# Kernel optimization log

Hardware: AMD Instinct MI355X
Metric: run time of the kernel (lower is better)

## Reference

```python
import math
import jax, jax.numpy as jnp
import numpy as np

B, S, D, H = 8, 1024, 1024, 16
P_DROP = 0.1  # dropout prob p used in forward
NEG_INF = -1e20


def setup_inputs() -> dict:
    key = jax.random.key(0)
    kq, kk, kv, km, kd = jax.random.split(key, 5)
    query = jax.random.normal(kq, (B, S, D), dtype=jnp.float32)
    key_t = jax.random.normal(kk, (B, S, D), dtype=jnp.float32)
    value = jax.random.normal(kv, (B, S, D), dtype=jnp.float32)
    mask = jax.random.randint(km, (B, S), 0, 2, dtype=jnp.int32)
    # Bernoulli keep-mask, as produced by an external dropout layer
    dropout_mask = (jax.random.uniform(kd, (B * H, S, S)) > P_DROP).astype(jnp.float32)
    return {"query": query, "key": key_t, "value": value,
            "mask": mask, "dropout_mask": dropout_mask}


def reference(query, key, value, mask, dropout_mask):
    b, q_len, dim = query.shape
    k_len = key.shape[1]
    dph = dim // H
    scale = math.sqrt(dph)

    def split_heads(t):  # [b, s, dim] -> [b, H, s, dph]
        return t.reshape(b, t.shape[1], H, dph).transpose(0, 2, 1, 3)

    q = split_heads(query) / scale
    k = split_heads(key)
    v = split_heads(value)

    # [b, H, q, k]
    scores = jnp.einsum('bhqd,bhkd->bhqk', q, k)
    attn_mask = (mask == 0)[:, None, None, :]  # [b,1,1,k]
    scores = jnp.where(attn_mask, NEG_INF, scores)

    # softmax in float32, cast back to query dtype
    weights = jax.nn.softmax(scores.astype(jnp.float32), axis=-1).astype(query.dtype)
    weights = weights * dropout_mask.reshape(b, H, q_len, k_len) * (1.0 / (1.0 - P_DROP))

    out = jnp.einsum('bhqk,bhkd->bhqd', weights, v)  # [b,H,q,dph]
    return out.transpose(0, 2, 1, 3).reshape(b, q_len, dim)
```

## Files before the change

### kernel.cpp

```cpp
#include <hip/hip_runtime.h>

namespace {
constexpr int Bn = 8;
constexpr int Sn = 1024;
constexpr int Dn = 1024;
constexpr int Hn = 16;
constexpr int DPH = 64;
constexpr int QB  = 64;
constexpr int KB  = 64;
constexpr float QSCALE    = 0.125f;
constexpr float DROPSCALE = 1.0f / 0.9f;

typedef __attribute__((ext_vector_type(4))) float    f32x4;
typedef __attribute__((ext_vector_type(8))) _Float16 f16x8;
typedef __attribute__((ext_vector_type(4))) _Float16 f16x4;
}

__global__ __launch_bounds__(256)
void mha_fwd(const float* __restrict__ Q, const float* __restrict__ K,
             const float* __restrict__ V, const int* __restrict__ msk,
             const float* __restrict__ dmask, float* __restrict__ out)
{
    __shared__ __align__(16) _Float16 Ql[QB][DPH + 8];
    __shared__ __align__(16) _Float16 Kl[KB][DPH + 8];
    __shared__ __align__(16) _Float16 Vt[DPH][KB + 8];
    __shared__ __align__(16) _Float16 Pl[4][16][KB + 8];

    const int tid = threadIdx.x;
    const int w   = tid >> 6;
    const int l   = tid & 63;
    const int fr  = l & 15;
    const int kg  = (l >> 4) << 3;
    const int rg  = (l >> 4) << 2;

    const int bid = blockIdx.x;
    const int qt = bid & (Sn / QB - 1);
    const int h  = (bid >> 4) & (Hn - 1);
    const int b  = bid >> 8;
    const int qbase = qt * QB;

    {
        const int row = tid >> 2;
        const int seg = (tid & 3) << 4;
        const float4* gq = reinterpret_cast<const float4*>(
            Q + ((size_t)(b * Sn + qbase + row)) * Dn + h * DPH + seg);
        #pragma unroll
        for (int i = 0; i < 4; ++i) {
            float4 v = gq[i];
            f16x4 qp;
            qp[0] = (_Float16)(v.x * QSCALE);
            qp[1] = (_Float16)(v.y * QSCALE);
            qp[2] = (_Float16)(v.z * QSCALE);
            qp[3] = (_Float16)(v.w * QSCALE);
            *reinterpret_cast<f16x4*>(&Ql[row][seg + i * 4]) = qp;
        }
    }
    __syncthreads();

    f16x8 qf0 = *reinterpret_cast<const f16x8*>(&Ql[w * 16 + fr][kg]);
    f16x8 qf1 = *reinterpret_cast<const f16x8*>(&Ql[w * 16 + fr][32 + kg]);

    f32x4 acc[4];
    #pragma unroll
    for (int dt = 0; dt < 4; ++dt) acc[dt] = (f32x4){0.f, 0.f, 0.f, 0.f};
    float m_r[4] = {-INFINITY, -INFINITY, -INFINITY, -INFINITY};
    float l_r[4] = {0.f, 0.f, 0.f, 0.f};

    const float* dm_base = dmask + ((size_t)(b * Hn + h)) * Sn * Sn
                         + (size_t)(qbase + w * 16) * Sn;

    #pragma unroll 1
    for (int kt = 0; kt < Sn / KB; ++kt) {
        __syncthreads();
        {
            const int row = tid >> 2;
            const int seg = (tid & 3) << 4;
            const size_t goff = ((size_t)(b * Sn + kt * KB + row)) * Dn + h * DPH + seg;
            const float4* gk = reinterpret_cast<const float4*>(K + goff);
            const float4* gv = reinterpret_cast<const float4*>(V + goff);
            #pragma unroll
            for (int i = 0; i < 4; ++i) {
                float4 kv = gk[i];
                f16x4 kp;
                kp[0] = (_Float16)kv.x; kp[1] = (_Float16)kv.y;
                kp[2] = (_Float16)kv.z; kp[3] = (_Float16)kv.w;
                *reinterpret_cast<f16x4*>(&Kl[row][seg + i * 4]) = kp;
                float4 vv = gv[i];
                Vt[seg + i * 4 + 0][row] = (_Float16)vv.x;
                Vt[seg + i * 4 + 1][row] = (_Float16)vv.y;
                Vt[seg + i * 4 + 2][row] = (_Float16)vv.z;
                Vt[seg + i * 4 + 3][row] = (_Float16)vv.w;
            }
        }
        __syncthreads();

        f32x4 sc[4];
        #pragma unroll
        for (int ct = 0; ct < 4; ++ct) {
            f16x8 kf0 = *reinterpret_cast<const f16x8*>(&Kl[ct * 16 + fr][kg]);
            f16x8 kf1 = *reinterpret_cast<const f16x8*>(&Kl[ct * 16 + fr][32 + kg]);
            f32x4 z = {0.f, 0.f, 0.f, 0.f};
            z = __builtin_amdgcn_mfma_f32_16x16x32_f16(qf0, kf0, z, 0, 0, 0);
            z = __builtin_amdgcn_mfma_f32_16x16x32_f16(qf1, kf1, z, 0, 0, 0);
            sc[ct] = z;
        }
        #pragma unroll
        for (int ct = 0; ct < 4; ++ct) {
            if (msk[b * Sn + kt * KB + ct * 16 + fr] == 0) {
                #pragma unroll
                for (int r = 0; r < 4; ++r) sc[ct][r] = -1e20f;
            }
        }
        float tm[4];
        #pragma unroll
        for (int r = 0; r < 4; ++r)
            tm[r] = fmaxf(fmaxf(sc[0][r], sc[1][r]), fmaxf(sc[2][r], sc[3][r]));
        #pragma unroll
        for (int off = 1; off < 16; off <<= 1) {
            #pragma unroll
            for (int r = 0; r < 4; ++r)
                tm[r] = fmaxf(tm[r], __shfl_xor(tm[r], off));
        }
        float al[4];
        #pragma unroll
        for (int r = 0; r < 4; ++r) {
            float mn = fmaxf(m_r[r], tm[r]);
            al[r] = __expf(m_r[r] - mn);
            m_r[r] = mn;
        }
        float p[4][4];
        float rs[4] = {0.f, 0.f, 0.f, 0.f};
        #pragma unroll
        for (int ct = 0; ct < 4; ++ct) {
            #pragma unroll
            for (int r = 0; r < 4; ++r) {
                p[ct][r] = __expf(sc[ct][r] - m_r[r]);
                rs[r] += p[ct][r];
            }
        }
        #pragma unroll
        for (int off = 1; off < 16; off <<= 1) {
            #pragma unroll
            for (int r = 0; r < 4; ++r)
                rs[r] += __shfl_xor(rs[r], off);
        }
        #pragma unroll
        for (int r = 0; r < 4; ++r)
            l_r[r] = l_r[r] * al[r] + rs[r];
        #pragma unroll
        for (int dt = 0; dt < 4; ++dt) {
            #pragma unroll
            for (int r = 0; r < 4; ++r) acc[dt][r] *= al[r];
        }
        #pragma unroll
        for (int r = 0; r < 4; ++r) {
            const float* dmrow = dm_base + (size_t)(rg + r) * Sn + kt * KB;
            #pragma unroll
            for (int ct = 0; ct < 4; ++ct) {
                float pd = p[ct][r] * dmrow[ct * 16 + fr];
                Pl[w][rg + r][ct * 16 + fr] = (_Float16)pd;
            }
        }
        f16x8 pf0 = *reinterpret_cast<const f16x8*>(&Pl[w][fr][kg]);
        f16x8 pf1 = *reinterpret_cast<const f16x8*>(&Pl[w][fr][32 + kg]);
        #pragma unroll
        for (int dt = 0; dt < 4; ++dt) {
            f16x8 vf0 = *reinterpret_cast<const f16x8*>(&Vt[dt * 16 + fr][kg]);
            f16x8 vf1 = *reinterpret_cast<const f16x8*>(&Vt[dt * 16 + fr][32 + kg]);
            acc[dt] = __builtin_amdgcn_mfma_f32_16x16x32_f16(pf0, vf0, acc[dt], 0, 0, 0);
            acc[dt] = __builtin_amdgcn_mfma_f32_16x16x32_f16(pf1, vf1, acc[dt], 0, 0, 0);
        }
    }

    #pragma unroll
    for (int r = 0; r < 4; ++r) {
        float inv = DROPSCALE / l_r[r];
        float* orow = out + ((size_t)(b * Sn + qbase + w * 16 + rg + r)) * Dn + h * DPH;
        #pragma unroll
        for (int dt = 0; dt < 4; ++dt)
            orow[dt * 16 + fr] = acc[dt][r] * inv;
    }
}

extern "C" void kernel_launch(void* const* d_in, const int* in_sizes, int n_in,
                              void* d_out, int out_size, void* d_ws, size_t ws_size,
                              hipStream_t stream)
{
    (void)in_sizes; (void)n_in; (void)out_size; (void)d_ws; (void)ws_size;
    const float* Q   = (const float*)d_in[0];
    const float* K   = (const float*)d_in[1];
    const float* V   = (const float*)d_in[2];
    const int*   msk = (const int*)d_in[3];
    const float* dm  = (const float*)d_in[4];
    float* o = (float*)d_out;

    dim3 grid(Bn * Hn * (Sn / QB));
    dim3 block(256);
    mha_fwd<<<grid, block, 0, stream>>>(Q, K, V, msk, dm, o);
}
```

Measured before the change: 976.8 us.

## Prefetch next K/V, mask and dropout tiles into registers; use exp2

Software-pipelines the loop. The next K/V tile, key mask and dropout-mask values are loaded into registers while the current tile is computed, hiding global memory latency behind the MFMA and softmax work. Q is loaded straight into MFMA fragments instead of going through LDS, and the exp calls become native v_exp_f32 with log2e folded into the Q scale. Launch bounds now request 4 blocks per CU, and the dropout multiply is done in fp16. These add register pressure that may cap occupancy, and fp16 products lose a little precision.

```diff
diff --git a/kernel.cpp b/kernel.cpp
--- a/kernel.cpp
+++ b/kernel.cpp
@@ -8,20 +8,27 @@
 constexpr int DPH = 64;
 constexpr int QB  = 64;
 constexpr int KB  = 64;
-constexpr float QSCALE    = 0.125f;
+constexpr int NT  = Sn / KB;
+constexpr float QSCALE    = 0.125f * 1.44269504088896340736f;
 constexpr float DROPSCALE = 1.0f / 0.9f;
 
 typedef __attribute__((ext_vector_type(4))) float    f32x4;
 typedef __attribute__((ext_vector_type(8))) _Float16 f16x8;
 typedef __attribute__((ext_vector_type(4))) _Float16 f16x4;
-}
-
-__global__ __launch_bounds__(256)
+typedef __attribute__((ext_vector_type(2))) _Float16 f16x2;
+}
+
+__device__ __forceinline__ float exp2_fast(float x) {
+    float r;
+    asm("v_exp_f32 %0, %1" : "=v"(r) : "v"(x));
+    return r;
+}
+
+__global__ __launch_bounds__(256, 4)
 void mha_fwd(const float* __restrict__ Q, const float* __restrict__ K,
              const float* __restrict__ V, const int* __restrict__ msk,
              const float* __restrict__ dmask, float* __restrict__ out)
 {
-    __shared__ __align__(16) _Float16 Ql[QB][DPH + 8];
     __shared__ __align__(16) _Float16 Kl[KB][DPH + 8];
     __shared__ __align__(16) _Float16 Vt[DPH][KB + 8];
     __shared__ __align__(16) _Float16 Pl[4][16][KB + 8];
@@ -39,26 +46,72 @@
     const int b  = bid >> 8;
     const int qbase = qt * QB;
 
+    f16x8 qf0, qf1;
     {
-        const int row = tid >> 2;
-        const int seg = (tid & 3) << 4;
-        const float4* gq = reinterpret_cast<const float4*>(
-            Q + ((size_t)(b * Sn + qbase + row)) * Dn + h * DPH + seg);
+        const float* qp = Q + ((size_t)(b * Sn + qbase + w * 16 + fr)) * Dn + h * DPH;
+        float4 a0 = *reinterpret_cast<const float4*>(qp + kg);
+        float4 a1 = *reinterpret_cast<const float4*>(qp + kg + 4);
+        float4 b0 = *reinterpret_cast<const float4*>(qp + 32 + kg);
+        float4 b1 = *reinterpret_cast<const float4*>(qp + 32 + kg + 4);
+        qf0[0] = (_Float16)(a0.x * QSCALE); qf0[1] = (_Float16)(a0.y * QSCALE);
+        qf0[2] = (_Float16)(a0.z * QSCALE); qf0[3] = (_Float16)(a0.w * QSCALE);
+        qf0[4] = (_Float16)(a1.x * QSCALE); qf0[5] = (_Float16)(a1.y * QSCALE);
+        qf0[6] = (_Float16)(a1.z * QSCALE); qf0[7] = (_Float16)(a1.w * QSCALE);
+        qf1[0] = (_Float16)(b0.x * QSCALE); qf1[1] = (_Float16)(b0.y * QSCALE);
+        qf1[2] = (_Float16)(b0.z * QSCALE); qf1[3] = (_Float16)(b0.w * QSCALE);
+        qf1[4] = (_Float16)(b1.x * QSCALE); qf1[5] = (_Float16)(b1.y * QSCALE);
+        qf1[6] = (_Float16)(b1.z * QSCALE); qf1[7] = (_Float16)(b1.w * QSCALE);
+    }
+
+    const int srow = tid >> 2;
+    const int sseg = (tid & 3) << 4;
+    float4 kreg[4], vreg[4];
+    int    mcur[4], mnxt[4];
+    f16x2  dmh[8];
+
+    const float* dm_base = dmask + ((size_t)(b * Hn + h)) * Sn * Sn
+                         + (size_t)(qbase + w * 16) * Sn;
+
+    auto kv_load = [&](int kt) {
+        const size_t goff = ((size_t)(b * Sn + kt * KB + srow)) * Dn + h * DPH + sseg;
+        const float4* gk = reinterpret_cast<const float4*>(K + goff);
+        const float4* gv = reinterpret_cast<const float4*>(V + goff);
+        #pragma unroll
+        for (int i = 0; i < 4; ++i) { kreg[i] = gk[i]; vreg[i] = gv[i]; }
+    };
+    auto kv_store = [&]() {
         #pragma unroll
         for (int i = 0; i < 4; ++i) {
-            float4 v = gq[i];
-            f16x4 qp;
-            qp[0] = (_Float16)(v.x * QSCALE);
-            qp[1] = (_Float16)(v.y * QSCALE);
-            qp[2] = (_Float16)(v.z * QSCALE);
-            qp[3] = (_Float16)(v.w * QSCALE);
-            *reinterpret_cast<f16x4*>(&Ql[row][seg + i * 4]) = qp;
-        }
-    }
-    __syncthreads();
-
-    f16x8 qf0 = *reinterpret_cast<const f16x8*>(&Ql[w * 16 + fr][kg]);
-    f16x8 qf1 = *reinterpret_cast<const f16x8*>(&Ql[w * 16 + fr][32 + kg]);
+            f16x4 kp;
+            kp[0] = (_Float16)kreg[i].x; kp[1] = (_Float16)kreg[i].y;
+            kp[2] = (_Float16)kreg[i].z; kp[3] = (_Float16)kreg[i].w;
+            *reinterpret_cast<f16x4*>(&Kl[srow][sseg + i * 4]) = kp;
+            Vt[sseg + i * 4 + 0][srow] = (_Float16)vreg[i].x;
+            Vt[sseg + i * 4 + 1][srow] = (_Float16)vreg[i].y;
+            Vt[sseg + i * 4 + 2][srow] = (_Float16)vreg[i].z;
+            Vt[sseg + i * 4 + 3][srow] = (_Float16)vreg[i].w;
+        }
+    };
+    auto dm_load = [&](int kt) {
+        #pragma unroll
+        for (int r = 0; r < 4; ++r) {
+            const float* dmrow = dm_base + (size_t)(rg + r) * Sn + kt * KB;
+            #pragma unroll
+            for (int ct = 0; ct < 4; ++ct) {
+                const int idx = r * 4 + ct;
+                dmh[idx >> 1][idx & 1] = (_Float16)dmrow[ct * 16 + fr];
+            }
+        }
+    };
+    auto msk_load = [&](int kt, int* dst) {
+        #pragma unroll
+        for (int ct = 0; ct < 4; ++ct)
+            dst[ct] = msk[b * Sn + kt * KB + ct * 16 + fr];
+    };
+
+    kv_load(0);
+    dm_load(0);
+    msk_load(0, mcur);
 
     f32x4 acc[4];
     #pragma unroll
@@ -66,31 +119,13 @@
     float m_r[4] = {-INFINITY, -INFINITY, -INFINITY, -INFINITY};
     float l_r[4] = {0.f, 0.f, 0.f, 0.f};
 
-    const float* dm_base = dmask + ((size_t)(b * Hn + h)) * Sn * Sn
-                         + (size_t)(qbase + w * 16) * Sn;
-
     #pragma unroll 1
-    for (int kt = 0; kt < Sn / KB; ++kt) {
+    for (int kt = 0; kt < NT; ++kt) {
         __syncthreads();
-        {
-            const int row = tid >> 2;
-            const int seg = (tid & 3) << 4;
-            const size_t goff = ((size_t)(b * Sn + kt * KB + row)) * Dn + h * DPH + seg;
-            const float4* gk = reinterpret_cast<const float4*>(K + goff);
-            const float4* gv = reinterpret_cast<const float4*>(V + goff);
-            #pragma unroll
-            for (int i = 0; i < 4; ++i) {
-                float4 kv = gk[i];
-                f16x4 kp;
-                kp[0] = (_Float16)kv.x; kp[1] = (_Float16)kv.y;
-                kp[2] = (_Float16)kv.z; kp[3] = (_Float16)kv.w;
-                *reinterpret_cast<f16x4*>(&Kl[row][seg + i * 4]) = kp;
-                float4 vv = gv[i];
-                Vt[seg + i * 4 + 0][row] = (_Float16)vv.x;
-                Vt[seg + i * 4 + 1][row] = (_Float16)vv.y;
-                Vt[seg + i * 4 + 2][row] = (_Float16)vv.z;
-                Vt[seg + i * 4 + 3][row] = (_Float16)vv.w;
-            }
+        kv_store();
+        if (kt + 1 < NT) {
+            kv_load(kt + 1);
+            msk_load(kt + 1, mnxt);
         }
         __syncthreads();
 
@@ -106,7 +141,7 @@
         }
         #pragma unroll
         for (int ct = 0; ct < 4; ++ct) {
-            if (msk[b * Sn + kt * KB + ct * 16 + fr] == 0) {
+            if (mcur[ct] == 0) {
                 #pragma unroll
                 for (int r = 0; r < 4; ++r) sc[ct][r] = -1e20f;
             }
@@ -125,7 +160,7 @@
         #pragma unroll
         for (int r = 0; r < 4; ++r) {
             float mn = fmaxf(m_r[r], tm[r]);
-            al[r] = __expf(m_r[r] - mn);
+            al[r] = exp2_fast(m_r[r] - mn);
             m_r[r] = mn;
         }
         float p[4][4];
@@ -134,7 +169,7 @@
         for (int ct = 0; ct < 4; ++ct) {
             #pragma unroll
             for (int r = 0; r < 4; ++r) {
-                p[ct][r] = __expf(sc[ct][r] - m_r[r]);
+                p[ct][r] = exp2_fast(sc[ct][r] - m_r[r]);
                 rs[r] += p[ct][r];
             }
         }
@@ -154,13 +189,14 @@
         }
         #pragma unroll
         for (int r = 0; r < 4; ++r) {
-            const float* dmrow = dm_base + (size_t)(rg + r) * Sn + kt * KB;
             #pragma unroll
             for (int ct = 0; ct < 4; ++ct) {
-                float pd = p[ct][r] * dmrow[ct * 16 + fr];
-                Pl[w][rg + r][ct * 16 + fr] = (_Float16)pd;
-            }
-        }
+                const int idx = r * 4 + ct;
+                _Float16 ph = (_Float16)p[ct][r] * dmh[idx >> 1][idx & 1];
+                Pl[w][rg + r][ct * 16 + fr] = ph;
+            }
+        }
+        if (kt + 1 < NT) dm_load(kt + 1);
         f16x8 pf0 = *reinterpret_cast<const f16x8*>(&Pl[w][fr][kg]);
         f16x8 pf1 = *reinterpret_cast<const f16x8*>(&Pl[w][fr][32 + kg]);
         #pragma unroll
@@ -170,6 +206,8 @@
             acc[dt] = __builtin_amdgcn_mfma_f32_16x16x32_f16(pf0, vf0, acc[dt], 0, 0, 0);
             acc[dt] = __builtin_amdgcn_mfma_f32_16x16x32_f16(pf1, vf1, acc[dt], 0, 0, 0);
         }
+        #pragma unroll
+        for (int ct = 0; ct < 4; ++ct) mcur[ct] = mnxt[ct];
     }
 
     #pragma unroll
```

Measured after the change: 813.8 us. -16.7%, faster.

## Transpose MFMA operands, prefetch K/V and dropout mask in registers, use exp2

Applied to the files above, without the earlier changes.

Swaps the MFMA operand order so each lane owns one query row. That makes row max/sum reductions only two cross-lane shuffles and lets the dropout mask, key mask and output be accessed as contiguous float4 vectors. K/V tiles are prefetched into registers one iteration ahead, and the dropout mask is double-buffered two tiles ahead to overlap global loads with compute. Q is now loaded straight to registers and pre-scaled by log2(e) so the softmax can use raw v_exp_f32. The cost is higher register pressure, which may reduce occupancy.

```diff
diff --git a/kernel.cpp b/kernel.cpp
--- a/kernel.cpp
+++ b/kernel.cpp
@@ -8,12 +8,20 @@
 constexpr int DPH = 64;
 constexpr int QB  = 64;
 constexpr int KB  = 64;
-constexpr float QSCALE    = 0.125f;
+constexpr int NT  = Sn / KB;
+constexpr float QSCALE    = 0.125f * 1.44269504088896340736f;
 constexpr float DROPSCALE = 1.0f / 0.9f;
 
 typedef __attribute__((ext_vector_type(4))) float    f32x4;
+typedef __attribute__((ext_vector_type(4))) int      i32x4;
 typedef __attribute__((ext_vector_type(8))) _Float16 f16x8;
 typedef __attribute__((ext_vector_type(4))) _Float16 f16x4;
+}
+
+__device__ __forceinline__ float exp2_fast(float x) {
+    float r;
+    asm("v_exp_f32 %0, %1" : "=v"(r) : "v"(x));
+    return r;
 }
 
 __global__ __launch_bounds__(256)
@@ -21,7 +29,6 @@
              const float* __restrict__ V, const int* __restrict__ msk,
              const float* __restrict__ dmask, float* __restrict__ out)
 {
-    __shared__ __align__(16) _Float16 Ql[QB][DPH + 8];
     __shared__ __align__(16) _Float16 Kl[KB][DPH + 8];
     __shared__ __align__(16) _Float16 Vt[DPH][KB + 8];
     __shared__ __align__(16) _Float16 Pl[4][16][KB + 8];
@@ -29,156 +36,161 @@
     const int tid = threadIdx.x;
     const int w   = tid >> 6;
     const int l   = tid & 63;
-    const int fr  = l & 15;
-    const int kg  = (l >> 4) << 3;
-    const int rg  = (l >> 4) << 2;
+    const int c16 = l & 15;
+    const int g   = l >> 4;
+    const int kg  = g << 3;
 
     const int bid = blockIdx.x;
     const int qt = bid & (Sn / QB - 1);
     const int h  = (bid >> 4) & (Hn - 1);
     const int b  = bid >> 8;
     const int qbase = qt * QB;
-
+    const size_t hoff = (size_t)h * DPH;
+
+    f16x8 qf0, qf1;
     {
-        const int row = tid >> 2;
-        const int seg = (tid & 3) << 4;
-        const float4* gq = reinterpret_cast<const float4*>(
-            Q + ((size_t)(b * Sn + qbase + row)) * Dn + h * DPH + seg);
+        const float* qp = Q + ((size_t)(b * Sn + qbase + w * 16 + c16)) * Dn + hoff;
+        f32x4 a0 = *reinterpret_cast<const f32x4*>(qp + kg);
+        f32x4 a1 = *reinterpret_cast<const f32x4*>(qp + kg + 4);
+        f32x4 b0 = *reinterpret_cast<const f32x4*>(qp + 32 + kg);
+        f32x4 b1 = *reinterpret_cast<const f32x4*>(qp + 32 + kg + 4);
+        #pragma unroll
+        for (int j = 0; j < 4; ++j) {
+            qf0[j]     = (_Float16)(a0[j] * QSCALE);
+            qf0[4 + j] = (_Float16)(a1[j] * QSCALE);
+            qf1[j]     = (_Float16)(b0[j] * QSCALE);
+            qf1[4 + j] = (_Float16)(b1[j] * QSCALE);
+        }
+    }
+
+    f32x4 kreg[4], vreg[4];
+    auto kv_load = [&](int kt) {
+        const size_t rbase = (size_t)(b * Sn + kt * KB);
         #pragma unroll
         for (int i = 0; i < 4; ++i) {
-            float4 v = gq[i];
-            f16x4 qp;
-            qp[0] = (_Float16)(v.x * QSCALE);
-            qp[1] = (_Float16)(v.y * QSCALE);
-            qp[2] = (_Float16)(v.z * QSCALE);
-            qp[3] = (_Float16)(v.w * QSCALE);
-            *reinterpret_cast<f16x4*>(&Ql[row][seg + i * 4]) = qp;
-        }
-    }
-    __syncthreads();
-
-    f16x8 qf0 = *reinterpret_cast<const f16x8*>(&Ql[w * 16 + fr][kg]);
-    f16x8 qf1 = *reinterpret_cast<const f16x8*>(&Ql[w * 16 + fr][32 + kg]);
+            kreg[i] = *reinterpret_cast<const f32x4*>(
+                K + (rbase + 16 * w + 4 * g + i) * Dn + hoff + 4 * c16);
+            vreg[i] = *reinterpret_cast<const f32x4*>(
+                V + (rbase + 4 * c16 + i) * Dn + hoff + 16 * w + 4 * g);
+        }
+    };
+    auto kv_store = [&]() {
+        #pragma unroll
+        for (int i = 0; i < 4; ++i) {
+            f16x4 kp;
+            #pragma unroll
+            for (int j = 0; j < 4; ++j) kp[j] = (_Float16)kreg[i][j];
+            *reinterpret_cast<f16x4*>(&Kl[16 * w + 4 * g + i][4 * c16]) = kp;
+        }
+        #pragma unroll
+        for (int j = 0; j < 4; ++j) {
+            f16x4 vp;
+            #pragma unroll
+            for (int i = 0; i < 4; ++i) vp[i] = (_Float16)vreg[i][j];
+            *reinterpret_cast<f16x4*>(&Vt[16 * w + 4 * g + j][4 * c16]) = vp;
+        }
+    };
+
+    f32x4 dmA[4], dmB[4];
+    const float* dm_base = dmask + ((size_t)(b * Hn + h)) * Sn * Sn
+                         + (size_t)(qbase + 16 * w + c16) * Sn;
+    auto dm_load = [&](int kt, f32x4* dst) {
+        #pragma unroll
+        for (int c = 0; c < 4; ++c)
+            dst[c] = *reinterpret_cast<const f32x4*>(dm_base + (size_t)kt * KB + 16 * c + 4 * g);
+    };
+
+    kv_load(0);
+    dm_load(0, dmA);
+    dm_load(1, dmB);
 
     f32x4 acc[4];
     #pragma unroll
     for (int dt = 0; dt < 4; ++dt) acc[dt] = (f32x4){0.f, 0.f, 0.f, 0.f};
-    float m_r[4] = {-INFINITY, -INFINITY, -INFINITY, -INFINITY};
-    float l_r[4] = {0.f, 0.f, 0.f, 0.f};
-
-    const float* dm_base = dmask + ((size_t)(b * Hn + h)) * Sn * Sn
-                         + (size_t)(qbase + w * 16) * Sn;
+    float m_r = -INFINITY;
+    float l_r = 0.f;
 
     #pragma unroll 1
-    for (int kt = 0; kt < Sn / KB; ++kt) {
+    for (int kt = 0; kt < NT; ++kt) {
         __syncthreads();
-        {
-            const int row = tid >> 2;
-            const int seg = (tid & 3) << 4;
-            const size_t goff = ((size_t)(b * Sn + kt * KB + row)) * Dn + h * DPH + seg;
-            const float4* gk = reinterpret_cast<const float4*>(K + goff);
-            const float4* gv = reinterpret_cast<const float4*>(V + goff);
-            #pragma unroll
-            for (int i = 0; i < 4; ++i) {
-                float4 kv = gk[i];
-                f16x4 kp;
-                kp[0] = (_Float16)kv.x; kp[1] = (_Float16)kv.y;
-                kp[2] = (_Float16)kv.z; kp[3] = (_Float16)kv.w;
-                *reinterpret_cast<f16x4*>(&Kl[row][seg + i * 4]) = kp;
-                float4 vv = gv[i];
-                Vt[seg + i * 4 + 0][row] = (_Float16)vv.x;
-                Vt[seg + i * 4 + 1][row] = (_Float16)vv.y;
-                Vt[seg + i * 4 + 2][row] = (_Float16)vv.z;
-                Vt[seg + i * 4 + 3][row] = (_Float16)vv.w;
+        kv_store();
+        if (kt + 1 < NT) kv_load(kt + 1);
+        i32x4 mi[4];
+        #pragma unroll
+        for (int c = 0; c < 4; ++c)
+            mi[c] = *reinterpret_cast<const i32x4*>(msk + b * Sn + kt * KB + 16 * c + 4 * g);
+        __syncthreads();
+
+        f32x4 sc[4];
+        #pragma unroll
+        for (int c = 0; c < 4; ++c) {
+            f16x8 kf0 = *reinterpret_cast<const f16x8*>(&Kl[c * 16 + c16][kg]);
+            f16x8 kf1 = *reinterpret_cast<const f16x8*>(&Kl[c * 16 + c16][32 + kg]);
+            f32x4 z = {0.f, 0.f, 0.f, 0.f};
+            z = __builtin_amdgcn_mfma_f32_16x16x32_f16(kf0, qf0, z, 0, 0, 0);
+            z = __builtin_amdgcn_mfma_f32_16x16x32_f16(kf1, qf1, z, 0, 0, 0);
+            sc[c] = z;
+        }
+        #pragma unroll
+        for (int c = 0; c < 4; ++c) {
+            #pragma unroll
+            for (int r = 0; r < 4; ++r)
+                sc[c][r] = (mi[c][r] != 0) ? sc[c][r] : -1e20f;
+        }
+        float tm = fmaxf(fmaxf(fmaxf(sc[0][0], sc[0][1]), fmaxf(sc[0][2], sc[0][3])),
+                         fmaxf(fmaxf(sc[1][0], sc[1][1]), fmaxf(sc[1][2], sc[1][3])));
+        tm = fmaxf(tm, fmaxf(fmaxf(fmaxf(sc[2][0], sc[2][1]), fmaxf(sc[2][2], sc[2][3])),
+                             fmaxf(fmaxf(sc[3][0], sc[3][1]), fmaxf(sc[3][2], sc[3][3]))));
+        tm = fmaxf(tm, __shfl_xor(tm, 16));
+        tm = fmaxf(tm, __shfl_xor(tm, 32));
+        float mn = fmaxf(m_r, tm);
+        float al = exp2_fast(m_r - mn);
+        m_r = mn;
+        float rs = 0.f;
+        #pragma unroll
+        for (int c = 0; c < 4; ++c) {
+            #pragma unroll
+            for (int r = 0; r < 4; ++r) {
+                sc[c][r] = exp2_fast(sc[c][r] - mn);
+                rs += sc[c][r];
             }
         }
-        __syncthreads();
-
-        f32x4 sc[4];
-        #pragma unroll
-        for (int ct = 0; ct < 4; ++ct) {
-            f16x8 kf0 = *reinterpret_cast<const f16x8*>(&Kl[ct * 16 + fr][kg]);
-            f16x8 kf1 = *reinterpret_cast<const f16x8*>(&Kl[ct * 16 + fr][32 + kg]);
-            f32x4 z = {0.f, 0.f, 0.f, 0.f};
-            z = __builtin_amdgcn_mfma_f32_16x16x32_f16(qf0, kf0, z, 0, 0, 0);
-            z = __builtin_amdgcn_mfma_f32_16x16x32_f16(qf1, kf1, z, 0, 0, 0);
-            sc[ct] = z;
-        }
-        #pragma unroll
-        for (int ct = 0; ct < 4; ++ct) {
-            if (msk[b * Sn + kt * KB + ct * 16 + fr] == 0) {
-                #pragma unroll
-                for (int r = 0; r < 4; ++r) sc[ct][r] = -1e20f;
-            }
-        }
-        float tm[4];
-        #pragma unroll
-        for (int r = 0; r < 4; ++r)
-            tm[r] = fmaxf(fmaxf(sc[0][r], sc[1][r]), fmaxf(sc[2][r], sc[3][r]));
-        #pragma unroll
-        for (int off = 1; off < 16; off <<= 1) {
-            #pragma unroll
-            for (int r = 0; r < 4; ++r)
-                tm[r] = fmaxf(tm[r], __shfl_xor(tm[r], off));
-        }
-        float al[4];
-        #pragma unroll
-        for (int r = 0; r < 4; ++r) {
-            float mn = fmaxf(m_r[r], tm[r]);
-            al[r] = __expf(m_r[r] - mn);
-            m_r[r] = mn;
-        }
-        float p[4][4];
-        float rs[4] = {0.f, 0.f, 0.f, 0.f};
-        #pragma unroll
-        for (int ct = 0; ct < 4; ++ct) {
-            #pragma unroll
-            for (int r = 0; r < 4; ++r) {
-                p[ct][r] = __expf(sc[ct][r] - m_r[r]);
-                rs[r] += p[ct][r];
-            }
-        }
-        #pragma unroll
-        for (int off = 1; off < 16; off <<= 1) {
-            #pragma unroll
-            for (int r = 0; r < 4; ++r)
-                rs[r] += __shfl_xor(rs[r], off);
-        }
-        #pragma unroll
-        for (int r = 0; r < 4; ++r)
-            l_r[r] = l_r[r] * al[r] + rs[r];
+        rs += __shfl_xor(rs, 16);
+        rs += __shfl_xor(rs, 32);
+        l_r = l_r * al + rs;
         #pragma unroll
         for (int dt = 0; dt < 4; ++dt) {
             #pragma unroll
-            for (int r = 0; r < 4; ++r) acc[dt][r] *= al[r];
-        }
-        #pragma unroll
-        for (int r = 0; r < 4; ++r) {
-            const float* dmrow = dm_base + (size_t)(rg + r) * Sn + kt * KB;
-            #pragma unroll
-            for (int ct = 0; ct < 4; ++ct) {
-                float pd = p[ct][r] * dmrow[ct * 16 + fr];
-                Pl[w][rg + r][ct * 16 + fr] = (_Float16)pd;
-            }
-        }
-        f16x8 pf0 = *reinterpret_cast<const f16x8*>(&Pl[w][fr][kg]);
-        f16x8 pf1 = *reinterpret_cast<const f16x8*>(&Pl[w][fr][32 + kg]);
+            for (int r = 0; r < 4; ++r) acc[dt][r] *= al;
+        }
+        const f32x4* dmv = (kt & 1) ? dmB : dmA;
+        #pragma unroll
+        for (int c = 0; c < 4; ++c) {
+            f16x4 pw;
+            #pragma unroll
+            for (int r = 0; r < 4; ++r) pw[r] = (_Float16)(sc[c][r] * dmv[c][r]);
+            *reinterpret_cast<f16x4*>(&Pl[w][c16][16 * c + 4 * g]) = pw;
+        }
+        if (kt + 2 < NT) dm_load(kt + 2, (kt & 1) ? dmB : dmA);
+        f16x8 pf0 = *reinterpret_cast<const f16x8*>(&Pl[w][c16][kg]);
+        f16x8 pf1 = *reinterpret_cast<const f16x8*>(&Pl[w][c16][32 + kg]);
         #pragma unroll
         for (int dt = 0; dt < 4; ++dt) {
-            f16x8 vf0 = *reinterpret_cast<const f16x8*>(&Vt[dt * 16 + fr][kg]);
-            f16x8 vf1 = *reinterpret_cast<const f16x8*>(&Vt[dt * 16 + fr][32 + kg]);
-            acc[dt] = __builtin_amdgcn_mfma_f32_16x16x32_f16(pf0, vf0, acc[dt], 0, 0, 0);
-            acc[dt] = __builtin_amdgcn_mfma_f32_16x16x32_f16(pf1, vf1, acc[dt], 0, 0, 0);
+            f16x8 vf0 = *reinterpret_cast<const f16x8*>(&Vt[dt * 16 + c16][kg]);
+            f16x8 vf1 = *reinterpret_cast<const f16x8*>(&Vt[dt * 16 + c16][32 + kg]);
+            acc[dt] = __builtin_amdgcn_mfma_f32_16x16x32_f16(vf0, pf0, acc[dt], 0, 0, 0);
+            acc[dt] = __builtin_amdgcn_mfma_f32_16x16x32_f16(vf1, pf1, acc[dt], 0, 0, 0);
         }
     }
 
+    float inv = DROPSCALE / l_r;
+    float* orow = out + ((size_t)(b * Sn + qbase + 16 * w + c16)) * Dn + hoff;
     #pragma unroll
-    for (int r = 0; r < 4; ++r) {
-        float inv = DROPSCALE / l_r[r];
-        float* orow = out + ((size_t)(b * Sn + qbase + w * 16 + rg + r)) * Dn + h * DPH;
-        #pragma unroll
-        for (int dt = 0; dt < 4; ++dt)
-            orow[dt * 16 + fr] = acc[dt][r] * inv;
+    for (int dt = 0; dt < 4; ++dt) {
+        f32x4 o4;
+        #pragma unroll
+        for (int r = 0; r < 4; ++r) o4[r] = acc[dt][r] * inv;
+        *reinterpret_cast<f32x4*>(orow + dt * 16 + 4 * g) = o4;
     }
 }
 
```

Result: faster. 822.8 us (-15.8%).
